# Kernel tuning notes

Measured on AMD Instinct MI355X. Metric: run time of the kernel, lower is better.

## Reference

```python
import jax, jax.numpy as jnp
import numpy as np
import math

B, C, TC, H, W = 8, 256, 512, 48, 48
EPS = 1e-6

def setup_inputs() -> dict:
    key = jax.random.key(0)
    kx, kt, kq, kk, kv = jax.random.split(key, 5)
    x = jax.random.normal(kx, (B, C, H, W), dtype=jnp.float32)
    token = jax.random.normal(kt, (B, TC, H, W), dtype=jnp.float32)
    # xavier_uniform for 1x1 conv weights [out, in]
    def xavier(k, fan_out, fan_in):
        a = math.sqrt(6.0 / (fan_in + fan_out))
        return jax.random.uniform(k, (fan_out, fan_in), dtype=jnp.float32, minval=-a, maxval=a)
    Wq = xavier(kq, C, C)
    Wk = xavier(kk, C, TC)
    Wv = xavier(kv, C, TC)
    alpha = jnp.float32(0.5)  # nonzero so the attention path affects the output
    return {"x": x, "token": token, "Wq": Wq, "Wk": Wk, "Wv": Wv, "alpha": alpha}

def reference(x, token, Wq, Wk, Wv, alpha):
    # 1x1 convs == per-pixel GEMMs over the channel dim
    q = jnp.einsum('oc,bchw->bohw', Wq, x)       # [B,C,H,W]
    k = jnp.einsum('oc,bchw->bohw', Wk, token)   # [B,C,H,W]
    v = jnp.einsum('oc,bchw->bohw', Wv, token)   # [B,C,H,W]
    b, c, h, w = q.shape
    n = h * w
    qf = q.reshape(b, c, n).transpose(0, 2, 1)   # [B,N,C]
    kf = k.reshape(b, c, n)                      # [B,C,N]
    vf = v.reshape(b, c, n).transpose(0, 2, 1)   # [B,N,C]
    # cosine normalization over the channel dim (F.normalize with eps clamp)
    qn = qf / jnp.maximum(jnp.linalg.norm(qf, axis=-1, keepdims=True), EPS)
    kn = kf / jnp.maximum(jnp.linalg.norm(kf, axis=1, keepdims=True), EPS)
    attn = jnp.einsum('bnc,bcm->bnm', qn, kn) / math.sqrt(c)  # [B,N,N]
    attn = jax.nn.softmax(attn, axis=-1)
    out = jnp.einsum('bnm,bmc->bnc', attn, vf)   # [B,N,C]
    out = out.transpose(0, 2, 1).reshape(b, c, h, w)
    return x + alpha * out
```

## Files before the change

### kernel.cpp

```cpp
#include <hip/hip_runtime.h>

#define B_   8
#define C_   256
#define TC_  512
#define HW_  2304
#define EPS_ 1e-6f

typedef __bf16 bf16_t;
typedef __bf16 bf16x8 __attribute__((ext_vector_type(8)));
typedef __bf16 bf16x4_t __attribute__((ext_vector_type(4)));
typedef float  f32x4 __attribute__((ext_vector_type(4)));
typedef unsigned int  u32;
typedef long long     i64;
typedef unsigned char u8;

__device__ __forceinline__ void g2l16(const void* g, void* l) {
    __builtin_amdgcn_global_load_lds(
        (const __attribute__((address_space(1))) unsigned int*)g,
        (__attribute__((address_space(3))) unsigned int*)l, 16, 0, 0);
}

__device__ __forceinline__ u8 to_fp8(float v) {
    return (u8)(__builtin_amdgcn_cvt_pk_fp8_f32(v, v, 0, false) & 0xff);
}

__global__ __launch_bounds__(256)
void wfrag_kernel(const float* __restrict__ wq, const float* __restrict__ wk,
                  const float* __restrict__ wv,
                  bf16_t* __restrict__ oq, bf16_t* __restrict__ ok,
                  bf16_t* __restrict__ ov)
{
    const int fid = blockIdx.x * 4 + (threadIdx.x >> 6);
    const int lane = threadIdx.x & 63;
    const int l16 = lane & 15, quad = lane >> 4;

    const float* src; bf16_t* dst; int cin, f;
    if (fid < 128)      { src = wq; dst = oq; cin = C_;  f = fid; }
    else if (fid < 384) { src = wk; dst = ok; cin = TC_; f = fid - 128; }
    else                { src = wv; dst = ov; cin = TC_; f = fid - 384; }
    const int nks = cin / 32;
    const int ot = f / nks, ks = f % nks;

    const float* s = src + (size_t)(ot * 16 + l16) * cin + ks * 32 + quad * 8;
    float4 a = *(const float4*)(s);
    float4 b = *(const float4*)(s + 4);
    bf16x8 o;
    o[0] = (__bf16)a.x; o[1] = (__bf16)a.y; o[2] = (__bf16)a.z; o[3] = (__bf16)a.w;
    o[4] = (__bf16)b.x; o[5] = (__bf16)b.y; o[6] = (__bf16)b.z; o[7] = (__bf16)b.w;
    *(bf16x8*)(dst + (size_t)f * 512 + lane * 8) = o;
}

template<int CIN, bool DO_V>
__global__ __launch_bounds__(256, 4)
void convqkv_kernel(const float* __restrict__ X, const bf16_t* __restrict__ Wa,
                    const bf16_t* __restrict__ Wvp, u8* __restrict__ outA,
                    u8* __restrict__ outV)
{
    const int bid = blockIdx.x;
    const int b  = bid & 7;
    const int n0 = (bid >> 3) * 16;
    const int tid = threadIdx.x;
    const int wv = tid >> 6;
    const int lane = tid & 63;
    const int quad = lane >> 4, l16 = lane & 15;
    const int NKS = CIN / 32;

    __shared__ bf16_t T[16][CIN + 8];
    __shared__ float ssp[4][16];

    {
        const float* Xb = X + (size_t)b * CIN * HW_ + n0;
        const int cl = tid >> 2;
        const int n4 = (tid & 3) * 4;
#pragma unroll
        for (int cp = 0; cp < CIN; cp += 64) {
            float4 v = *(const float4*)(Xb + (size_t)(cp + cl) * HW_ + n4);
            T[n4 + 0][cp + cl] = (__bf16)v.x;
            T[n4 + 1][cp + cl] = (__bf16)v.y;
            T[n4 + 2][cp + cl] = (__bf16)v.z;
            T[n4 + 3][cp + cl] = (__bf16)v.w;
        }
    }
    __syncthreads();

    bf16x8 af[CIN / 32];
#pragma unroll
    for (int ks = 0; ks < CIN / 32; ks++)
        af[ks] = *(const bf16x8*)(&T[l16][ks * 32 + quad * 8]);

    const int ot0 = wv * 4;

    f32x4 accK[4];
#pragma unroll
    for (int p = 0; p < 4; p++) accK[p] = (f32x4){0.f, 0.f, 0.f, 0.f};
    {
        const bf16_t* wbase = Wa + ((size_t)ot0 * NKS) * 512 + lane * 8;
#pragma unroll
        for (int ks = 0; ks < CIN / 32; ks++)
#pragma unroll
            for (int p = 0; p < 4; p++) {
                bf16x8 bw = *(const bf16x8*)(wbase + (size_t)(p * NKS + ks) * 512);
                accK[p] = __builtin_amdgcn_mfma_f32_16x16x32_bf16(af[ks], bw, accK[p], 0, 0, 0);
            }
    }

    {
        float ssr[4];
#pragma unroll
        for (int r = 0; r < 4; r++) {
            float ss = accK[0][r] * accK[0][r] + accK[1][r] * accK[1][r]
                     + accK[2][r] * accK[2][r] + accK[3][r] * accK[3][r];
            ss += __shfl_xor(ss, 1);
            ss += __shfl_xor(ss, 2);
            ss += __shfl_xor(ss, 4);
            ss += __shfl_xor(ss, 8);
            ssr[r] = ss;
        }
        if (l16 == 0) {
#pragma unroll
            for (int r = 0; r < 4; r++) ssp[wv][quad * 4 + r] = ssr[r];
        }
    }

    f32x4 accV[4];
    if (DO_V) {
#pragma unroll
        for (int p = 0; p < 4; p++) accV[p] = (f32x4){0.f, 0.f, 0.f, 0.f};
        const bf16_t* wbase = Wvp + ((size_t)ot0 * NKS) * 512 + lane * 8;
#pragma unroll
        for (int ks = 0; ks < CIN / 32; ks++)
#pragma unroll
            for (int p = 0; p < 4; p++) {
                bf16x8 aw = *(const bf16x8*)(wbase + (size_t)(p * NKS + ks) * 512);
                accV[p] = __builtin_amdgcn_mfma_f32_16x16x32_bf16(aw, af[ks], accV[p], 0, 0, 0);
            }
    }

    __syncthreads();

    float scale[4];
#pragma unroll
    for (int r = 0; r < 4; r++) {
        int px = quad * 4 + r;
        float s = ssp[0][px] + ssp[1][px] + ssp[2][px] + ssp[3][px];
        scale[r] = 1.0f / fmaxf(sqrtf(s), EPS_);
    }
    {
        u8* oa = outA + ((size_t)b * HW_ + n0 + quad * 4) * C_ + l16;
#pragma unroll
        for (int p = 0; p < 4; p++)
#pragma unroll
            for (int r = 0; r < 4; r++)
                oa[(size_t)r * C_ + (ot0 + p) * 16] = to_fp8(accK[p][r] * scale[r]);
    }

    if (DO_V) {
#pragma unroll
        for (int p = 0; p < 4; p++)
#pragma unroll
            for (int r = 0; r < 4; r++)
                outV[((size_t)b * C_ + (ot0 + p) * 16 + quad * 4 + r) * HW_ + n0 + l16]
                    = to_fp8(accV[p][r]);
    }
}

__global__ __launch_bounds__(256, 4)
void attn_part_kernel(const u8* __restrict__ q8, const u8* __restrict__ k8,
                      const u8* __restrict__ v8,
                      bf16_t* __restrict__ Opart, float* __restrict__ lpart,
                      int tilesPerSplit, int JS)
{
    const int bid = blockIdx.x;
    const int b   = bid & 7;
    const int rr  = bid >> 3;
    const int js  = rr % JS;
    const int mt  = rr / JS;
    const int wv   = threadIdx.x >> 6;
    const int lane = threadIdx.x & 63;
    const int quad = lane >> 4;
    const int l16  = lane & 15;
    const int row0 = mt * 64 + wv * 16;
    const int jbase = js * tilesPerSplit * 32;

    const u8* qb = q8 + (size_t)b * HW_ * C_;
    const u8* kb = k8 + (size_t)b * HW_ * C_;
    const u8* vb = v8 + (size_t)b * C_ * HW_;

    __shared__ u8 Kbuf[2][8192];
    __shared__ u8 Vbuf[2][8192];

    i64 aq[8];
    {
        const u8* r0 = qb + (size_t)(row0 + l16) * C_ + quad * 8;
#pragma unroll
        for (int t = 0; t < 8; t++) aq[t] = *(const i64*)(r0 + t * 32);
    }

    f32x4 O[16];
#pragma unroll
    for (int i = 0; i < 16; i++) O[i] = (f32x4){0.f, 0.f, 0.f, 0.f};
    float lsum = 0.f;

    const int kj = lane & 31;
    const int kh = lane >> 5;
    const int vg = (lane & 1) ^ ((lane >> 3) & 1);
    const int vc = lane >> 1;

#define STAGE(bufi, j0g)                                                       \
    {                                                                          \
        _Pragma("unroll")                                                      \
        for (int p = 0; p < 2; p++) {                                          \
            int i = wv * 2 + p;                                                \
            int s = i * 2 + kh;                                                \
            g2l16(kb + (size_t)((j0g) + kj) * C_ + s * 16,                     \
                  &Kbuf[bufi][i * 1024]);                                      \
        }                                                                      \
        _Pragma("unroll")                                                      \
        for (int p = 0; p < 2; p++) {                                          \
            int i = wv * 2 + p;                                                \
            int c = i * 32 + vc;                                               \
            g2l16(vb + (size_t)c * HW_ + (j0g) + vg * 16,                      \
                  &Vbuf[bufi][i * 1024]);                                      \
        }                                                                      \
    }

    STAGE(0, jbase)

    const int koff  = (quad >> 1) * 512 + l16 * 16 + (quad & 1) * 8;
    const int vbase = l16 * 32 + ((((quad >> 1) ^ (l16 >> 2)) & 1) << 4)
                    + (quad & 1) * 8;

    for (int tt = 0; tt < tilesPerSplit; tt++) {
        __syncthreads();
        if (tt + 1 < tilesPerSplit) STAGE((tt + 1) & 1, jbase + (tt + 1) * 32)

        const u8* Kb = Kbuf[tt & 1];
        const u8* Vb = Vbuf[tt & 1];

        f32x4 s00 = (f32x4){0.f,0.f,0.f,0.f}, s01 = (f32x4){0.f,0.f,0.f,0.f};
#pragma unroll
        for (int t = 0; t < 8; t++) {
            i64 bk0 = *(const i64*)(Kb + t * 1024 + koff);
            i64 bk1 = *(const i64*)(Kb + t * 1024 + koff + 256);
            s00 = __builtin_amdgcn_mfma_f32_16x16x32_fp8_fp8(bk0, aq[t], s00, 0, 0, 0);
            s01 = __builtin_amdgcn_mfma_f32_16x16x32_fp8_fp8(bk1, aq[t], s01, 0, 0, 0);
        }

        float pA0 = __expf(s00[0] * 0.0625f), pA1 = __expf(s00[1] * 0.0625f);
        float pA2 = __expf(s00[2] * 0.0625f), pA3 = __expf(s00[3] * 0.0625f);
        float pB0 = __expf(s01[0] * 0.0625f), pB1 = __expf(s01[1] * 0.0625f);
        float pB2 = __expf(s01[2] * 0.0625f), pB3 = __expf(s01[3] * 0.0625f);
        lsum += (pA0 + pA1 + pA2 + pA3) + (pB0 + pB1 + pB2 + pB3);

        u32 A = __builtin_amdgcn_cvt_pk_fp8_f32(pA0, pA1, 0, false);
        A     = __builtin_amdgcn_cvt_pk_fp8_f32(pA2, pA3, A, true);
        u32 Bw = __builtin_amdgcn_cvt_pk_fp8_f32(pB0, pB1, 0, false);
        Bw     = __builtin_amdgcn_cvt_pk_fp8_f32(pB2, pB3, Bw, true);

        asm volatile("v_permlane32_swap_b32 %0, %1" : "+v"(A), "+v"(Bw));
        asm volatile("v_permlane16_swap_b32 %0, %1" : "+v"(A), "+v"(Bw));
        i64 ap0 = ((i64)(u32)Bw << 32) | (i64)A;

#pragma unroll
        for (int ct = 0; ct < 16; ct++) {
            i64 bv = *(const i64*)(Vb + ct * 512 + vbase);
            O[ct] = __builtin_amdgcn_mfma_f32_16x16x32_fp8_fp8(ap0, bv, O[ct], 0, 0, 0);
        }
    }

    lsum += __shfl_xor(lsum, 16);
    lsum += __shfl_xor(lsum, 32);
    float* lp = lpart + (size_t)(js * B_ + b) * HW_;
    if (quad == 0) lp[row0 + l16] = lsum;

    bf16_t* op = Opart + (size_t)(js * B_ + b) * C_ * HW_;
#pragma unroll
    for (int ct = 0; ct < 16; ct++) {
        int c = ct * 16 + l16;
        bf16x4_t v0;
        v0[0] = (__bf16)O[ct][0]; v0[1] = (__bf16)O[ct][1];
        v0[2] = (__bf16)O[ct][2]; v0[3] = (__bf16)O[ct][3];
        *(bf16x4_t*)(op + (size_t)c * HW_ + row0 + quad * 4) = v0;
    }
#undef STAGE
}

__global__ __launch_bounds__(256)
void epilogue_kernel(const float* __restrict__ x, const bf16_t* __restrict__ Opart,
                     const float* __restrict__ lpart, const float* __restrict__ alphaPtr,
                     float* __restrict__ out, int JS)
{
    const float a = *alphaPtr;
    const size_t S = (size_t)B_ * C_ * HW_;
    size_t flat = ((size_t)blockIdx.x * 256 + threadIdx.x) * 4;
    int bc = (int)(flat / HW_);
    int n  = (int)(flat % HW_);
    int b  = bc >> 8;
    float4 xv = *(const float4*)(x + flat);
    float s0 = 0.f, s1 = 0.f, s2 = 0.f, s3 = 0.f;
    float l0 = 0.f, l1 = 0.f, l2 = 0.f, l3 = 0.f;
    for (int js = 0; js < JS; js++) {
        bf16x4_t ov = *(const bf16x4_t*)(Opart + (size_t)js * S + flat);
        s0 += (float)ov[0]; s1 += (float)ov[1];
        s2 += (float)ov[2]; s3 += (float)ov[3];
        float4 lv = *(const float4*)(lpart + (size_t)(js * B_ + b) * HW_ + n);
        l0 += lv.x; l1 += lv.y; l2 += lv.z; l3 += lv.w;
    }
    float4 r;
    r.x = xv.x + a * s0 / l0;
    r.y = xv.y + a * s1 / l1;
    r.z = xv.z + a * s2 / l2;
    r.w = xv.w + a * s3 / l3;
    *(float4*)(out + flat) = r;
}

extern "C" void kernel_launch(void* const* d_in, const int* in_sizes, int n_in,
                              void* d_out, int out_size, void* d_ws, size_t ws_size,
                              hipStream_t stream)
{
    (void)in_sizes; (void)n_in; (void)out_size;
    const float* x     = (const float*)d_in[0];
    const float* token = (const float*)d_in[1];
    const float* Wq    = (const float*)d_in[2];
    const float* Wk    = (const float*)d_in[3];
    const float* Wv    = (const float*)d_in[4];
    const float* alpha = (const float*)d_in[5];
    float* out = (float*)d_out;

    const size_t S = (size_t)B_ * HW_ * C_;

    int JS = 4;
    for (;;) {
        size_t need = (12 + 2 * (size_t)JS) * S
                    + (size_t)JS * B_ * HW_ * 4 + (size_t)B_ * HW_ * 4;
        if (need <= ws_size || JS == 1) break;
        JS >>= 1;
    }
    const int tilesPerSplit = (HW_ / 32) / JS;

    char* ws = (char*)d_ws;
    bf16_t* WqL   = (bf16_t*)(ws + 6 * S);
    bf16_t* WkL   = WqL + (size_t)C_ * C_;
    bf16_t* WvL   = WkL + (size_t)C_ * TC_;
    u8*     q8    = (u8*)(ws + 7 * S);
    u8*     k8    = (u8*)(ws + 8 * S);
    u8*     v8    = (u8*)(ws + 9 * S);
    bf16_t* Opart = (bf16_t*)(ws + 12 * S);
    float*  lpart = (float*)(ws + (12 + 2 * (size_t)JS) * S);

    wfrag_kernel<<<dim3(160), dim3(256), 0, stream>>>(Wq, Wk, Wv, WqL, WkL, WvL);
    convqkv_kernel<C_,  false><<<dim3(B_ * HW_ / 16), dim3(256), 0, stream>>>(x,     WqL, nullptr, q8, nullptr);
    convqkv_kernel<TC_, true ><<<dim3(B_ * HW_ / 16), dim3(256), 0, stream>>>(token, WkL, WvL,     k8, v8);
    attn_part_kernel<<<dim3(JS * B_ * (HW_ / 64)), dim3(256), 0, stream>>>(q8, k8, v8, Opart, lpart, tilesPerSplit, JS);
    epilogue_kernel<<<dim3((int)(S / 1024)), dim3(256), 0, stream>>>(x, Opart, lpart, alpha, out, JS);
}
```

Measured before the change: 222.6 us.

## Fuse attention split-K and epilogue into one kernel with in-block wave reduction

Replaces the split-KV attention kernel plus separate epilogue with one fused kernel. Each block handles 16 query rows, and its four waves each process an interleaved quarter of the key tiles. Partial outputs are reduced through shared memory, then the kernel normalizes and writes x + alpha*out directly. This removes the bf16 partial-output round trip through global memory and one kernel launch. In exchange, K/V are now read straight from global memory with no LDS staging or double buffering. Each block also re-reads all of K and V for only 16 rows, which raises global/L2 traffic and latency exposure.

```diff
diff --git a/kernel.cpp b/kernel.cpp
--- a/kernel.cpp
+++ b/kernel.cpp
@@ -8,17 +8,10 @@
 
 typedef __bf16 bf16_t;
 typedef __bf16 bf16x8 __attribute__((ext_vector_type(8)));
-typedef __bf16 bf16x4_t __attribute__((ext_vector_type(4)));
 typedef float  f32x4 __attribute__((ext_vector_type(4)));
 typedef unsigned int  u32;
 typedef long long     i64;
 typedef unsigned char u8;
-
-__device__ __forceinline__ void g2l16(const void* g, void* l) {
-    __builtin_amdgcn_global_load_lds(
-        (const __attribute__((address_space(1))) unsigned int*)g,
-        (__attribute__((address_space(3))) unsigned int*)l, 16, 0, 0);
-}
 
 __device__ __forceinline__ u8 to_fp8(float v) {
     return (u8)(__builtin_amdgcn_cvt_pk_fp8_f32(v, v, 0, false) & 0xff);
@@ -164,36 +157,31 @@
     }
 }
 
-__global__ __launch_bounds__(256, 4)
-void attn_part_kernel(const u8* __restrict__ q8, const u8* __restrict__ k8,
-                      const u8* __restrict__ v8,
-                      bf16_t* __restrict__ Opart, float* __restrict__ lpart,
-                      int tilesPerSplit, int JS)
+__global__ __launch_bounds__(256, 3)
+void attn_fused_kernel(const u8* __restrict__ q8, const u8* __restrict__ k8,
+                       const u8* __restrict__ v8, const float* __restrict__ x,
+                       const float* __restrict__ alphaPtr, float* __restrict__ out)
 {
     const int bid = blockIdx.x;
     const int b   = bid & 7;
-    const int rr  = bid >> 3;
-    const int js  = rr % JS;
-    const int mt  = rr / JS;
+    const int n0  = (bid >> 3) * 16;
     const int wv   = threadIdx.x >> 6;
     const int lane = threadIdx.x & 63;
     const int quad = lane >> 4;
     const int l16  = lane & 15;
-    const int row0 = mt * 64 + wv * 16;
-    const int jbase = js * tilesPerSplit * 32;
 
     const u8* qb = q8 + (size_t)b * HW_ * C_;
     const u8* kb = k8 + (size_t)b * HW_ * C_;
     const u8* vb = v8 + (size_t)b * C_ * HW_;
 
-    __shared__ u8 Kbuf[2][8192];
-    __shared__ u8 Vbuf[2][8192];
+    __shared__ float Rb[2][16][260];
+    __shared__ float lsb[4][16];
 
     i64 aq[8];
     {
-        const u8* r0 = qb + (size_t)(row0 + l16) * C_ + quad * 8;
-#pragma unroll
-        for (int t = 0; t < 8; t++) aq[t] = *(const i64*)(r0 + t * 32);
+        const u8* qr = qb + (size_t)(n0 + l16) * C_ + quad * 8;
+#pragma unroll
+        for (int t = 0; t < 8; t++) aq[t] = *(const i64*)(qr + t * 32);
     }
 
     f32x4 O[16];
@@ -201,47 +189,18 @@
     for (int i = 0; i < 16; i++) O[i] = (f32x4){0.f, 0.f, 0.f, 0.f};
     float lsum = 0.f;
 
-    const int kj = lane & 31;
-    const int kh = lane >> 5;
-    const int vg = (lane & 1) ^ ((lane >> 3) & 1);
-    const int vc = lane >> 1;
-
-#define STAGE(bufi, j0g)                                                       \
-    {                                                                          \
-        _Pragma("unroll")                                                      \
-        for (int p = 0; p < 2; p++) {                                          \
-            int i = wv * 2 + p;                                                \
-            int s = i * 2 + kh;                                                \
-            g2l16(kb + (size_t)((j0g) + kj) * C_ + s * 16,                     \
-                  &Kbuf[bufi][i * 1024]);                                      \
-        }                                                                      \
-        _Pragma("unroll")                                                      \
-        for (int p = 0; p < 2; p++) {                                          \
-            int i = wv * 2 + p;                                                \
-            int c = i * 32 + vc;                                               \
-            g2l16(vb + (size_t)c * HW_ + (j0g) + vg * 16,                      \
-                  &Vbuf[bufi][i * 1024]);                                      \
-        }                                                                      \
-    }
-
-    STAGE(0, jbase)
-
-    const int koff  = (quad >> 1) * 512 + l16 * 16 + (quad & 1) * 8;
-    const int vbase = l16 * 32 + ((((quad >> 1) ^ (l16 >> 2)) & 1) << 4)
-                    + (quad & 1) * 8;
-
-    for (int tt = 0; tt < tilesPerSplit; tt++) {
-        __syncthreads();
-        if (tt + 1 < tilesPerSplit) STAGE((tt + 1) & 1, jbase + (tt + 1) * 32)
-
-        const u8* Kb = Kbuf[tt & 1];
-        const u8* Vb = Vbuf[tt & 1];
+#pragma unroll 1
+    for (int s = 0; s < HW_ / 128; s++) {
+        const int j0 = (s * 4 + wv) * 32;
+        const u8* kr0 = kb + (size_t)(j0 + l16) * C_ + quad * 8;
+        const u8* kr1 = kr0 + 16 * C_;
+        const u8* vr  = vb + (size_t)l16 * HW_ + j0 + quad * 8;
 
         f32x4 s00 = (f32x4){0.f,0.f,0.f,0.f}, s01 = (f32x4){0.f,0.f,0.f,0.f};
 #pragma unroll
         for (int t = 0; t < 8; t++) {
-            i64 bk0 = *(const i64*)(Kb + t * 1024 + koff);
-            i64 bk1 = *(const i64*)(Kb + t * 1024 + koff + 256);
+            i64 bk0 = *(const i64*)(kr0 + t * 32);
+            i64 bk1 = *(const i64*)(kr1 + t * 32);
             s00 = __builtin_amdgcn_mfma_f32_16x16x32_fp8_fp8(bk0, aq[t], s00, 0, 0, 0);
             s01 = __builtin_amdgcn_mfma_f32_16x16x32_fp8_fp8(bk1, aq[t], s01, 0, 0, 0);
         }
@@ -252,8 +211,8 @@
         float pB2 = __expf(s01[2] * 0.0625f), pB3 = __expf(s01[3] * 0.0625f);
         lsum += (pA0 + pA1 + pA2 + pA3) + (pB0 + pB1 + pB2 + pB3);
 
-        u32 A = __builtin_amdgcn_cvt_pk_fp8_f32(pA0, pA1, 0, false);
-        A     = __builtin_amdgcn_cvt_pk_fp8_f32(pA2, pA3, A, true);
+        u32 A  = __builtin_amdgcn_cvt_pk_fp8_f32(pA0, pA1, 0, false);
+        A      = __builtin_amdgcn_cvt_pk_fp8_f32(pA2, pA3, A, true);
         u32 Bw = __builtin_amdgcn_cvt_pk_fp8_f32(pB0, pB1, 0, false);
         Bw     = __builtin_amdgcn_cvt_pk_fp8_f32(pB2, pB3, Bw, true);
 
@@ -263,62 +222,66 @@
 
 #pragma unroll
         for (int ct = 0; ct < 16; ct++) {
-            i64 bv = *(const i64*)(Vb + ct * 512 + vbase);
+            i64 bv = *(const i64*)(vr + (size_t)ct * 16 * HW_);
             O[ct] = __builtin_amdgcn_mfma_f32_16x16x32_fp8_fp8(ap0, bv, O[ct], 0, 0, 0);
         }
     }
 
     lsum += __shfl_xor(lsum, 16);
     lsum += __shfl_xor(lsum, 32);
-    float* lp = lpart + (size_t)(js * B_ + b) * HW_;
-    if (quad == 0) lp[row0 + l16] = lsum;
-
-    bf16_t* op = Opart + (size_t)(js * B_ + b) * C_ * HW_;
-#pragma unroll
-    for (int ct = 0; ct < 16; ct++) {
-        int c = ct * 16 + l16;
-        bf16x4_t v0;
-        v0[0] = (__bf16)O[ct][0]; v0[1] = (__bf16)O[ct][1];
-        v0[2] = (__bf16)O[ct][2]; v0[3] = (__bf16)O[ct][3];
-        *(bf16x4_t*)(op + (size_t)c * HW_ + row0 + quad * 4) = v0;
-    }
-#undef STAGE
-}
-
-__global__ __launch_bounds__(256)
-void epilogue_kernel(const float* __restrict__ x, const bf16_t* __restrict__ Opart,
-                     const float* __restrict__ lpart, const float* __restrict__ alphaPtr,
-                     float* __restrict__ out, int JS)
-{
+    if (quad == 0) lsb[wv][l16] = lsum;
+
+    if (wv & 1) {
+        float (*R)[260] = Rb[wv >> 1];
+#pragma unroll
+        for (int ct = 0; ct < 16; ct++)
+#pragma unroll
+            for (int r = 0; r < 4; r++)
+                R[quad * 4 + r][ct * 16 + l16] = O[ct][r];
+    }
+    __syncthreads();
+    if (!(wv & 1)) {
+        float (*R)[260] = Rb[wv >> 1];
+#pragma unroll
+        for (int ct = 0; ct < 16; ct++)
+#pragma unroll
+            for (int r = 0; r < 4; r++) {
+                float v = O[ct][r] + R[quad * 4 + r][ct * 16 + l16];
+                R[quad * 4 + r][ct * 16 + l16] = v;
+            }
+    }
+    __syncthreads();
+
     const float a = *alphaPtr;
-    const size_t S = (size_t)B_ * C_ * HW_;
-    size_t flat = ((size_t)blockIdx.x * 256 + threadIdx.x) * 4;
-    int bc = (int)(flat / HW_);
-    int n  = (int)(flat % HW_);
-    int b  = bc >> 8;
-    float4 xv = *(const float4*)(x + flat);
-    float s0 = 0.f, s1 = 0.f, s2 = 0.f, s3 = 0.f;
-    float l0 = 0.f, l1 = 0.f, l2 = 0.f, l3 = 0.f;
-    for (int js = 0; js < JS; js++) {
-        bf16x4_t ov = *(const bf16x4_t*)(Opart + (size_t)js * S + flat);
-        s0 += (float)ov[0]; s1 += (float)ov[1];
-        s2 += (float)ov[2]; s3 += (float)ov[3];
-        float4 lv = *(const float4*)(lpart + (size_t)(js * B_ + b) * HW_ + n);
-        l0 += lv.x; l1 += lv.y; l2 += lv.z; l3 += lv.w;
-    }
-    float4 r;
-    r.x = xv.x + a * s0 / l0;
-    r.y = xv.y + a * s1 / l1;
-    r.z = xv.z + a * s2 / l2;
-    r.w = xv.w + a * s3 / l3;
-    *(float4*)(out + flat) = r;
+    float lt[4];
+#pragma unroll
+    for (int r = 0; r < 4; r++) {
+        int row = quad * 4 + r;
+        lt[r] = lsb[0][row] + lsb[1][row] + lsb[2][row] + lsb[3][row];
+    }
+    const float* xb = x   + (size_t)b * C_ * HW_ + n0;
+    float*       ob = out + (size_t)b * C_ * HW_ + n0;
+#pragma unroll
+    for (int ci = 0; ci < 4; ci++) {
+        int ct = wv * 4 + ci;
+        int c  = ct * 16 + l16;
+        f32x4 xv = *(const f32x4*)(xb + (size_t)c * HW_ + quad * 4);
+        f32x4 rv;
+#pragma unroll
+        for (int r = 0; r < 4; r++) {
+            float ov = Rb[0][quad * 4 + r][ct * 16 + l16]
+                     + Rb[1][quad * 4 + r][ct * 16 + l16];
+            rv[r] = xv[r] + a * ov / lt[r];
+        }
+        *(f32x4*)(ob + (size_t)c * HW_ + quad * 4) = rv;
+    }
 }
 
 extern "C" void kernel_launch(void* const* d_in, const int* in_sizes, int n_in,
                               void* d_out, int out_size, void* d_ws, size_t ws_size,
                               hipStream_t stream)
 {
-    (void)in_sizes; (void)n_in; (void)out_size;
+    (void)in_sizes; (void)n_in; (void)out_size; (void)ws_size;
     const float* x     = (const float*)d_in[0];
     const float* token = (const float*)d_in[1];
     const float* Wq    = (const float*)d_in[2];
@@ -329,28 +292,16 @@
 
     const size_t S = (size_t)B_ * HW_ * C_;
 
-    int JS = 4;
-    for (;;) {
-        size_t need = (12 + 2 * (size_t)JS) * S
-                    + (size_t)JS * B_ * HW_ * 4 + (size_t)B_ * HW_ * 4;
-        if (need <= ws_size || JS == 1) break;
-        JS >>= 1;
-    }
-    const int tilesPerSplit = (HW_ / 32) / JS;
-
     char* ws = (char*)d_ws;
-    bf16_t* WqL   = (bf16_t*)(ws + 6 * S);
-    bf16_t* WkL   = WqL + (size_t)C_ * C_;
-    bf16_t* WvL   = WkL + (size_t)C_ * TC_;
-    u8*     q8    = (u8*)(ws + 7 * S);
-    u8*     k8    = (u8*)(ws + 8 * S);
-    u8*     v8    = (u8*)(ws + 9 * S);
-    bf16_t* Opart = (bf16_t*)(ws + 12 * S);
-    float*  lpart = (float*)(ws + (12 + 2 * (size_t)JS) * S);
+    bf16_t* WqL = (bf16_t*)(ws + 6 * S);
+    bf16_t* WkL = WqL + (size_t)C_ * C_;
+    bf16_t* WvL = WkL + (size_t)C_ * TC_;
+    u8*     q8  = (u8*)(ws + 7 * S);
+    u8*     k8  = (u8*)(ws + 8 * S);
+    u8*     v8  = (u8*)(ws + 9 * S);
 
     wfrag_kernel<<<dim3(160), dim3(256), 0, stream>>>(Wq, Wk, Wv, WqL, WkL, WvL);
     convqkv_kernel<C_,  false><<<dim3(B_ * HW_ / 16), dim3(256), 0, stream>>>(x,     WqL, nullptr, q8, nullptr);
     convqkv_kernel<TC_, true ><<<dim3(B_ * HW_ / 16), dim3(256), 0, stream>>>(token, WkL, WvL,     k8, v8);
-    attn_part_kernel<<<dim3(JS * B_ * (HW_ / 64)), dim3(256), 0, stream>>>(q8, k8, v8, Opart, lpart, tilesPerSplit, JS);
-    epilogue_kernel<<<dim3((int)(S / 1024)), dim3(256), 0, stream>>>(x, Opart, lpart, alpha, out, JS);
-}
+    attn_fused_kernel<<<dim3(B_ * HW_ / 16), dim3(256), 0, stream>>>(q8, k8, v8, x, alpha, out);
+}
```

Result: slower. 519.3 us (+133.3%).

## Triple-buffer K/V tiles with explicit vmcnt waits and MFMA priority

Applied to the files above, without the earlier changes.

Moves the attention partial kernel from double to triple buffering of K/V LDS tiles, prefetching two tiles ahead. It replaces __syncthreads with a partial s_waitcnt vmcnt plus s_barrier so loads stay in flight across iterations. It also simplifies the LDS staging layout (row-major 32-byte rows, dropping the XOR swizzle) and raises wave priority around the MFMA loops. In exchange, LDS use grows to 48KB per block, launch bounds drop to 3 blocks per CU, and the unswizzled layout may cause bank conflicts.

```diff
diff --git a/kernel.cpp b/kernel.cpp
--- a/kernel.cpp
+++ b/kernel.cpp
@@ -164,7 +164,7 @@
     }
 }
 
-__global__ __launch_bounds__(256, 4)
+__global__ __launch_bounds__(256, 3)
 void attn_part_kernel(const u8* __restrict__ q8, const u8* __restrict__ k8,
                       const u8* __restrict__ v8,
                       bf16_t* __restrict__ Opart, float* __restrict__ lpart,
@@ -186,8 +186,8 @@
     const u8* kb = k8 + (size_t)b * HW_ * C_;
     const u8* vb = v8 + (size_t)b * C_ * HW_;
 
-    __shared__ u8 Kbuf[2][8192];
-    __shared__ u8 Vbuf[2][8192];
+    __shared__ u8 Kbuf[3][8192];
+    __shared__ u8 Vbuf[3][8192];
 
     i64 aq[8];
     {
@@ -201,50 +201,54 @@
     for (int i = 0; i < 16; i++) O[i] = (f32x4){0.f, 0.f, 0.f, 0.f};
     float lsum = 0.f;
 
-    const int kj = lane & 31;
-    const int kh = lane >> 5;
-    const int vg = (lane & 1) ^ ((lane >> 3) & 1);
-    const int vc = lane >> 1;
+    const int rl = lane >> 1;
+    const int ch = lane & 1;
 
 #define STAGE(bufi, j0g)                                                       \
     {                                                                          \
         _Pragma("unroll")                                                      \
         for (int p = 0; p < 2; p++) {                                          \
             int i = wv * 2 + p;                                                \
-            int s = i * 2 + kh;                                                \
-            g2l16(kb + (size_t)((j0g) + kj) * C_ + s * 16,                     \
+            g2l16(kb + (size_t)((j0g) + rl) * C_ + i * 32 + ch * 16,           \
                   &Kbuf[bufi][i * 1024]);                                      \
         }                                                                      \
         _Pragma("unroll")                                                      \
         for (int p = 0; p < 2; p++) {                                          \
             int i = wv * 2 + p;                                                \
-            int c = i * 32 + vc;                                               \
-            g2l16(vb + (size_t)c * HW_ + (j0g) + vg * 16,                      \
+            g2l16(vb + (size_t)(i * 32 + rl) * HW_ + (j0g) + ch * 16,          \
                   &Vbuf[bufi][i * 1024]);                                      \
         }                                                                      \
     }
 
     STAGE(0, jbase)
-
-    const int koff  = (quad >> 1) * 512 + l16 * 16 + (quad & 1) * 8;
-    const int vbase = l16 * 32 + ((((quad >> 1) ^ (l16 >> 2)) & 1) << 4)
-                    + (quad & 1) * 8;
+    STAGE(1, jbase + 32)
+
+    const int koff = l16 * 32 + quad * 8;
 
     for (int tt = 0; tt < tilesPerSplit; tt++) {
-        __syncthreads();
-        if (tt + 1 < tilesPerSplit) STAGE((tt + 1) & 1, jbase + (tt + 1) * 32)
-
-        const u8* Kb = Kbuf[tt & 1];
-        const u8* Vb = Vbuf[tt & 1];
+        if (tt + 1 < tilesPerSplit) {
+            asm volatile("s_waitcnt vmcnt(4)" ::: "memory");
+        } else {
+            asm volatile("s_waitcnt vmcnt(0)" ::: "memory");
+        }
+        __builtin_amdgcn_s_barrier();
+        if (tt + 2 < tilesPerSplit)
+            STAGE((tt + 2) % 3, jbase + (tt + 2) * 32)
+        __builtin_amdgcn_sched_barrier(0);
+
+        const u8* Kb = Kbuf[tt % 3];
+        const u8* Vb = Vbuf[tt % 3];
 
         f32x4 s00 = (f32x4){0.f,0.f,0.f,0.f}, s01 = (f32x4){0.f,0.f,0.f,0.f};
+        __builtin_amdgcn_s_setprio(1);
 #pragma unroll
         for (int t = 0; t < 8; t++) {
             i64 bk0 = *(const i64*)(Kb + t * 1024 + koff);
-            i64 bk1 = *(const i64*)(Kb + t * 1024 + koff + 256);
+            i64 bk1 = *(const i64*)(Kb + t * 1024 + koff + 512);
             s00 = __builtin_amdgcn_mfma_f32_16x16x32_fp8_fp8(bk0, aq[t], s00, 0, 0, 0);
             s01 = __builtin_amdgcn_mfma_f32_16x16x32_fp8_fp8(bk1, aq[t], s01, 0, 0, 0);
         }
+        __builtin_amdgcn_s_setprio(0);
 
         float pA0 = __expf(s00[0] * 0.0625f), pA1 = __expf(s00[1] * 0.0625f);
         float pA2 = __expf(s00[2] * 0.0625f), pA3 = __expf(s00[3] * 0.0625f);
@@ -252,8 +256,8 @@
         float pB2 = __expf(s01[2] * 0.0625f), pB3 = __expf(s01[3] * 0.0625f);
         lsum += (pA0 + pA1 + pA2 + pA3) + (pB0 + pB1 + pB2 + pB3);
 
-        u32 A = __builtin_amdgcn_cvt_pk_fp8_f32(pA0, pA1, 0, false);
-        A     = __builtin_amdgcn_cvt_pk_fp8_f32(pA2, pA3, A, true);
+        u32 A  = __builtin_amdgcn_cvt_pk_fp8_f32(pA0, pA1, 0, false);
+        A      = __builtin_amdgcn_cvt_pk_fp8_f32(pA2, pA3, A, true);
         u32 Bw = __builtin_amdgcn_cvt_pk_fp8_f32(pB0, pB1, 0, false);
         Bw     = __builtin_amdgcn_cvt_pk_fp8_f32(pB2, pB3, Bw, true);
 
@@ -261,11 +265,13 @@
         asm volatile("v_permlane16_swap_b32 %0, %1" : "+v"(A), "+v"(Bw));
         i64 ap0 = ((i64)(u32)Bw << 32) | (i64)A;
 
+        __builtin_amdgcn_s_setprio(1);
 #pragma unroll
         for (int ct = 0; ct < 16; ct++) {
-            i64 bv = *(const i64*)(Vb + ct * 512 + vbase);
+            i64 bv = *(const i64*)(Vb + ct * 512 + koff);
             O[ct] = __builtin_amdgcn_mfma_f32_16x16x32_fp8_fp8(ap0, bv, O[ct], 0, 0, 0);
         }
+        __builtin_amdgcn_s_setprio(0);
     }
 
     lsum += __shfl_xor(lsum, 16);
```

Result: slower. 248.1 us (+11.5%).
